# Optimization experiments

Measured on AMD Instinct MI355X. Metric: run time of the kernel, lower is better.

## Reference

```python
import jax, jax.numpy as jnp
import numpy as np

N_NODES = 50000
N_EDGES = 1600000
IN_FEAT = 256
HIDDEN = 128
N_CLASSES = 16


def gcn_conv(x, edge_index, W, b, n_nodes):
    """PyG GCNConv: x' = D^{-1/2} (A+I) D^{-1/2} (x @ W) + b."""
    h = x @ W  # project first (PyG order), messages are in out_dim
    src, dst = edge_index[0], edge_index[1]
    loops = jnp.arange(n_nodes, dtype=src.dtype)
    src = jnp.concatenate([src, loops])
    dst = jnp.concatenate([dst, loops])
    # degree of A+I (count incoming edges incl. self loop)
    deg = jax.ops.segment_sum(jnp.ones_like(dst, dtype=h.dtype), dst, num_segments=n_nodes)
    dis = jax.lax.rsqrt(deg)  # deg >= 1 thanks to self loops
    norm = dis[src] * dis[dst]  # [E+N]
    msgs = h[src] * norm[:, None]  # gather + scale
    out = jax.ops.segment_sum(msgs, dst, num_segments=n_nodes)  # scatter-add
    return out + b


def setup_inputs() -> dict:
    key = jax.random.key(0)
    k_x, k_e, k_w1, k_b1, k_w2, k_b2 = jax.random.split(key, 6)
    x = jax.random.normal(k_x, (N_NODES, IN_FEAT), dtype=jnp.float32)
    edge_index = jax.random.randint(k_e, (2, N_EDGES), 0, N_NODES, dtype=jnp.int64)
    s1 = 1.0 / np.sqrt(IN_FEAT)
    s2 = 1.0 / np.sqrt(HIDDEN)
    W1 = jax.random.uniform(k_w1, (IN_FEAT, HIDDEN), jnp.float32, -s1, s1)
    b1 = jax.random.uniform(k_b1, (HIDDEN,), jnp.float32, -s1, s1)
    W2 = jax.random.uniform(k_w2, (HIDDEN, N_CLASSES), jnp.float32, -s2, s2)
    b2 = jax.random.uniform(k_b2, (N_CLASSES,), jnp.float32, -s2, s2)
    return {"x": x, "edge_index": edge_index, "W1": W1, "b1": b1, "W2": W2, "b2": b2}


def reference(x, edge_index, W1, b1, W2, b2):
    n = x.shape[0]
    h = gcn_conv(x, edge_index, W1, b1, n)
    h = jax.nn.relu(h)
    logits = gcn_conv(h, edge_index, W2, b2, n)
    return logits, jax.nn.softmax(logits, axis=1)
```

## Files before the change

kernel.cpp:

```cpp
#include <hip/hip_runtime.h>
#include <hip/hip_bf16.h>
#include <math.h>

#define N_NODES 50000
#define N_EDGES 1600000
#define IN_FEAT 256
#define HIDDEN 128
#define N_CLASSES 16

#define ECHUNK 2048
#define NCHK 782
#define NBKT 196
#define BCAP 10240
#define CSTR 16

typedef __attribute__((ext_vector_type(8))) short short8;
typedef __attribute__((ext_vector_type(4))) float floatx4;

__device__ __forceinline__ unsigned short f2bf(float f) {
    unsigned u = __float_as_uint(f);
    return (unsigned short)((u + 0x7fffu + ((u >> 16) & 1u)) >> 16);
}

__device__ __forceinline__ unsigned pk2bf(float a, float b) {
    __hip_bfloat162 h = __float22bfloat162_rn(make_float2(a, b));
    union { __hip_bfloat162 h; unsigned u; } cv;
    cv.h = h;
    return cv.u;
}

__device__ __forceinline__ float bflo(unsigned u) { return __uint_as_float(u << 16); }
__device__ __forceinline__ float bfhi(unsigned u) { return __uint_as_float(u & 0xffff0000u); }

__global__ __launch_bounds__(256) void scatter_edges2(const int* __restrict__ src,
                                                      const int* __restrict__ dst,
                                                      int* __restrict__ cursor,
                                                      unsigned int* __restrict__ sorted,
                                                      const float* __restrict__ W1,
                                                      unsigned short* __restrict__ w1t) {
    __shared__ int hloc[256];
    int t = threadIdx.x;
    hloc[t] = 0;
    if (blockIdx.x < HIDDEN)
        w1t[blockIdx.x * IN_FEAT + t] = f2bf(W1[t * HIDDEN + blockIdx.x]);
    __syncthreads();
    int base = blockIdx.x * ECHUNK;
    int end = min(base + ECHUNK, N_EDGES);
    for (int i = base + t; i < end; i += 256)
        atomicAdd(&hloc[dst[i] >> 8], 1);
    __syncthreads();
    int cnt = hloc[t];
    int lbase = 0;
    if (cnt > 0) lbase = t * BCAP + atomicAdd(&cursor[t * CSTR], cnt);
    __syncthreads();
    hloc[t] = lbase;
    __syncthreads();
    for (int i = base + t; i < end; i += 256) {
        int d = dst[i];
        int s = src[i];
        int pos = atomicAdd(&hloc[d >> 8], 1);
        sorted[pos] = ((unsigned)d << 16) | (unsigned)s;
    }
}

__global__ __launch_bounds__(512) void build_csr2(const unsigned int* __restrict__ sorted,
                                                  const int* __restrict__ cursor,
                                                  int* __restrict__ rs,
                                                  int* __restrict__ re,
                                                  float* __restrict__ dis,
                                                  unsigned short* __restrict__ csr_src) {
    __shared__ int cnt[256];
    __shared__ int roff[256];
    int t = threadIdx.x;
    int bkt = blockIdx.x;
    int ebase = bkt * BCAP;
    int eend = ebase + cursor[bkt * CSTR];
    if (t < 256) cnt[t] = 0;
    __syncthreads();
    for (int i = ebase + t; i < eend; i += 512)
        atomicAdd(&cnt[(sorted[i] >> 16) & 255], 1);
    __syncthreads();
    int v = 0;
    if (t < 256) { v = cnt[t]; roff[t] = v; }
    __syncthreads();
    for (int off = 1; off < 256; off <<= 1) {
        int x = (t < 256 && t >= off) ? roff[t - off] : 0;
        __syncthreads();
        if (t < 256) roff[t] += x;
        __syncthreads();
    }
    if (t < 256) {
        int excl = roff[t] - v;
        int node = bkt * 256 + t;
        if (node < N_NODES) {
            rs[node] = ebase + excl;
            re[node] = ebase + excl + v;
            dis[node] = 1.0f / sqrtf((float)(v + 1));
        }
        cnt[t] = ebase + excl;
    }
    __syncthreads();
    for (int i = ebase + t; i < eend; i += 512) {
        unsigned e = sorted[i];
        int pos = atomicAdd(&cnt[(e >> 16) & 255], 1);
        csr_src[pos] = (unsigned short)(e & 0xffffu);
    }
}

#define XCHDW 260
#define KBLK (4 * XCHDW)

__global__ __launch_bounds__(256) void gemm1_mfma(const float* __restrict__ x,
                                                  const unsigned short* __restrict__ w1t,
                                                  const float* __restrict__ dis,
                                                  unsigned int* __restrict__ g1) {
    __shared__ float xs[8 * KBLK];
    int tid = threadIdx.x;
    int w = tid >> 6;
    int lane = tid & 63;
    int quad = lane >> 4;
    int c = lane & 15;
    int row_base = blockIdx.x * 32;
    int col_base = w * 32;

    int st_row = min(row_base + 8 * w + (lane >> 3), N_NODES - 1);
    const float* gp1 = x + (size_t)st_row * IN_FEAT + (lane & 7) * 4;
#pragma unroll
    for (int kk = 0; kk < 8; ++kk)
        __builtin_amdgcn_global_load_lds(
            (const __attribute__((address_space(1))) void*)(gp1 + kk * 32),
            (__attribute__((address_space(3))) void*)&xs[kk * KBLK + w * XCHDW], 16, 0, 0);

    floatx4 acc[2][2] = {};
    const unsigned short* bp[2];
#pragma unroll
    for (int nt = 0; nt < 2; ++nt)
        bp[nt] = w1t + (size_t)(col_base + nt * 16 + c) * IN_FEAT + quad * 8;

    int dwoff[2];
#pragma unroll
    for (int rt = 0; rt < 2; ++rt) {
        int rit = rt * 16 + c;
        dwoff[rt] = (rit >> 3) * XCHDW + (rit & 7) * 32 + quad * 8;
    }

    __syncthreads();

#pragma unroll
    for (int kk = 0; kk < 8; ++kk) {
        short8 b[2];
#pragma unroll
        for (int nt = 0; nt < 2; ++nt)
            b[nt] = *(const short8*)(bp[nt] + kk * 32);
        short8 a[2];
#pragma unroll
        for (int rt = 0; rt < 2; ++rt) {
            float4 f0 = *(const float4*)&xs[kk * KBLK + dwoff[rt]];
            float4 f1 = *(const float4*)&xs[kk * KBLK + dwoff[rt] + 4];
            union { short8 s; unsigned u[4]; } au;
            au.u[0] = pk2bf(f0.x, f0.y);
            au.u[1] = pk2bf(f0.z, f0.w);
            au.u[2] = pk2bf(f1.x, f1.y);
            au.u[3] = pk2bf(f1.z, f1.w);
            a[rt] = au.s;
        }
#pragma unroll
        for (int rt = 0; rt < 2; ++rt)
#pragma unroll
            for (int nt = 0; nt < 2; ++nt)
                acc[rt][nt] = __builtin_amdgcn_mfma_f32_16x16x32_bf16(a[rt], b[nt], acc[rt][nt], 0, 0, 0);
    }

    bool evenlane = (lane & 1) == 0;
#pragma unroll
    for (int rt = 0; rt < 2; ++rt) {
#pragma unroll
        for (int reg = 0; reg < 4; ++reg) {
            int row = row_base + rt * 16 + quad * 4 + reg;
            float dv = dis[min(row, N_NODES - 1)];
#pragma unroll
            for (int nt = 0; nt < 2; ++nt) {
                float v = acc[rt][nt][reg] * dv;
                float vo = __shfl_xor(v, 1);
                if (evenlane && row < N_NODES) {
                    unsigned pkd = (unsigned)f2bf(v) | ((unsigned)f2bf(vo) << 16);
                    int col = col_base + nt * 16 + c;
                    g1[(size_t)(col >> 5) * (N_NODES * 16) + (size_t)row * 16 + ((col & 31) >> 1)] = pkd;
                }
            }
        }
    }
}

__global__ __launch_bounds__(256) void agg1_sliced(const uint4* __restrict__ g1,
                                                   const int* __restrict__ rs,
                                                   const int* __restrict__ re,
                                                   const unsigned short* __restrict__ csr_src,
                                                   const float* __restrict__ dis,
                                                   const float* __restrict__ b1,
                                                   const float* __restrict__ W2,
                                                   float* __restrict__ g2) {
    __shared__ float w2s[32 * 16];
    __shared__ float rbuf[4][16][36];
    int tid = threadIdx.x;
    int bi = blockIdx.x;
    int bucket = bi >> 4;
    int xcd = bi & 7;
    int slice = xcd >> 1;
    int quarter = ((bi >> 3) & 1) * 2 + (xcd & 1);

    for (int i = tid; i < 512; i += 256) w2s[i] = W2[slice * 512 + i];
    __syncthreads();

    int wave = tid >> 6, lane = tid & 63;
    int g = lane >> 2, m4 = lane & 3;
    const uint4* plane = g1 + (size_t)slice * (N_NODES * 4);
    int node = bucket * 256 + quarter * 64 + wave * 16 + g;
    bool alive = (node < N_NODES);
    float dvs = 0.f;

#define ACC8(u) do { a0 += bflo((u).x); a1 += bfhi((u).x); a2 += bflo((u).y); a3 += bfhi((u).y); \
                     a4 += bflo((u).z); a5 += bfhi((u).z); a6 += bflo((u).w); a7 += bfhi((u).w); } while (0)
#define GATH(IV, U0, U1, U2, U3) do {                       \
        int j0_ = (int)((IV).x & 0xffffu);                  \
        int j1_ = (int)((IV).x >> 16);                      \
        int j2_ = (int)((IV).y & 0xffffu);                  \
        int j3_ = (int)((IV).y >> 16);                      \
        U0 = plane[(size_t)j0_ * 4 + m4];                   \
        U1 = plane[(size_t)j1_ * 4 + m4];                   \
        U2 = plane[(size_t)j2_ * 4 + m4];                   \
        U3 = plane[(size_t)j3_ * 4 + m4];                   \
    } while (0)

    if (alive) {
        uint4 su = plane[(size_t)node * 4 + m4];
        float a0 = bflo(su.x), a1 = bfhi(su.x), a2 = bflo(su.y), a3 = bfhi(su.y);
        float a4 = bflo(su.z), a5 = bfhi(su.z), a6 = bflo(su.w), a7 = bfhi(su.w);
        int e = rs[node], e1v = re[node];
        while ((e & 3) && e < e1v) {
            int j = csr_src[e];
            uint4 u = plane[(size_t)j * 4 + m4];
            ACC8(u);
            ++e;
        }
        int nb = (e1v - e) >> 2;
        if (nb >= 2) {
            uint2 Ia = *(const uint2*)&csr_src[e];
            uint2 Ib = *(const uint2*)&csr_src[e + 4];
            uint4 A0, A1, A2, A3, B0, B1, B2, B3;
            GATH(Ia, A0, A1, A2, A3);
            GATH(Ib, B0, B1, B2, B3);
            __builtin_amdgcn_sched_barrier(0);
            int b = 2;
            while (b + 2 <= nb) {
                Ia = *(const uint2*)&csr_src[e + 4 * b];
                ACC8(A0); ACC8(A1); ACC8(A2); ACC8(A3);
                GATH(Ia, A0, A1, A2, A3);
                __builtin_amdgcn_sched_barrier(0);
                Ib = *(const uint2*)&csr_src[e + 4 * b + 4];
                ACC8(B0); ACC8(B1); ACC8(B2); ACC8(B3);
                GATH(Ib, B0, B1, B2, B3);
                __builtin_amdgcn_sched_barrier(0);
                b += 2;
            }
            int rem = nb - b;
            ACC8(A0); ACC8(A1); ACC8(A2); ACC8(A3);
            if (rem) {
                Ia = *(const uint2*)&csr_src[e + 4 * b];
                GATH(Ia, A0, A1, A2, A3);
            }
            ACC8(B0); ACC8(B1); ACC8(B2); ACC8(B3);
            if (rem) { ACC8(A0); ACC8(A1); ACC8(A2); ACC8(A3); }
            e += 4 * nb;
        } else if (nb >= 1) {
            uint2 Iv = *(const uint2*)&csr_src[e];
            uint4 U0, U1, U2, U3;
            GATH(Iv, U0, U1, U2, U3);
            ACC8(U0); ACC8(U1); ACC8(U2); ACC8(U3);
            e += 4;
        }
        while (e < e1v) {
            int j = csr_src[e];
            uint4 u = plane[(size_t)j * 4 + m4];
            ACC8(u);
            ++e;
        }

        float dv = dis[node];
        dvs = dv;
        float4 bb0 = *(const float4*)&b1[slice * 32 + 8 * m4];
        float4 bb1 = *(const float4*)&b1[slice * 32 + 8 * m4 + 4];
        float4 r0, r1;
        r0.x = fmaxf(fmaf(dv, a0, bb0.x), 0.f);
        r0.y = fmaxf(fmaf(dv, a1, bb0.y), 0.f);
        r0.z = fmaxf(fmaf(dv, a2, bb0.z), 0.f);
        r0.w = fmaxf(fmaf(dv, a3, bb0.w), 0.f);
        r1.x = fmaxf(fmaf(dv, a4, bb1.x), 0.f);
        r1.y = fmaxf(fmaf(dv, a5, bb1.y), 0.f);
        r1.z = fmaxf(fmaf(dv, a6, bb1.z), 0.f);
        r1.w = fmaxf(fmaf(dv, a7, bb1.w), 0.f);
        *(float4*)&rbuf[wave][g][8 * m4] = r0;
        *(float4*)&rbuf[wave][g][8 * m4 + 4] = r1;
    }
    __builtin_amdgcn_sched_barrier(0);
    if (alive) {
        float p0 = 0.f, p1 = 0.f, p2 = 0.f, p3 = 0.f;
#pragma unroll
        for (int fb = 0; fb < 8; ++fb) {
            float4 rv = *(const float4*)&rbuf[wave][g][fb * 4];
            float4 w0 = *(const float4*)&w2s[(fb * 4 + 0) * 16 + 4 * m4];
            float4 w1 = *(const float4*)&w2s[(fb * 4 + 1) * 16 + 4 * m4];
            float4 w2 = *(const float4*)&w2s[(fb * 4 + 2) * 16 + 4 * m4];
            float4 w3 = *(const float4*)&w2s[(fb * 4 + 3) * 16 + 4 * m4];
            p0 = fmaf(rv.x, w0.x, p0); p1 = fmaf(rv.x, w0.y, p1);
            p2 = fmaf(rv.x, w0.z, p2); p3 = fmaf(rv.x, w0.w, p3);
            p0 = fmaf(rv.y, w1.x, p0); p1 = fmaf(rv.y, w1.y, p1);
            p2 = fmaf(rv.y, w1.z, p2); p3 = fmaf(rv.y, w1.w, p3);
            p0 = fmaf(rv.z, w2.x, p0); p1 = fmaf(rv.z, w2.y, p1);
            p2 = fmaf(rv.z, w2.z, p2); p3 = fmaf(rv.z, w2.w, p3);
            p0 = fmaf(rv.w, w3.x, p0); p1 = fmaf(rv.w, w3.y, p1);
            p2 = fmaf(rv.w, w3.z, p2); p3 = fmaf(rv.w, w3.w, p3);
        }
        float* go = g2 + (size_t)node * 16 + 4 * m4;
        unsafeAtomicAdd(go + 0, dvs * p0);
        unsafeAtomicAdd(go + 1, dvs * p1);
        unsafeAtomicAdd(go + 2, dvs * p2);
        unsafeAtomicAdd(go + 3, dvs * p3);
    }
#undef GATH
#undef ACC8
}

__global__ __launch_bounds__(256) void agg2_softmax(const float4* __restrict__ g2,
                                                    const int* __restrict__ rs,
                                                    const int* __restrict__ re,
                                                    const unsigned short* __restrict__ csr_src,
                                                    const float* __restrict__ dis,
                                                    const float* __restrict__ b2,
                                                    float* __restrict__ out) {
    int tid = threadIdx.x;
    int wave = tid >> 6, lane = tid & 63;
    int g = lane >> 2, m4 = lane & 3;
    int node = blockIdx.x * 64 + wave * 16 + g;
    if (node >= N_NODES) return;

    float4 acc = g2[(size_t)node * 4 + m4];

#define ACC4(u) do { acc.x += (u).x; acc.y += (u).y; acc.z += (u).z; acc.w += (u).w; } while (0)
#define GATH4(IV, U0, U1, U2, U3) do {                      \
        int j0_ = (int)((IV).x & 0xffffu);                  \
        int j1_ = (int)((IV).x >> 16);                      \
        int j2_ = (int)((IV).y & 0xffffu);                  \
        int j3_ = (int)((IV).y >> 16);                      \
        U0 = g2[(size_t)j0_ * 4 + m4];                      \
        U1 = g2[(size_t)j1_ * 4 + m4];                      \
        U2 = g2[(size_t)j2_ * 4 + m4];                      \
        U3 = g2[(size_t)j3_ * 4 + m4];                      \
    } while (0)

    int e = rs[node], e1v = re[node];
    while ((e & 3) && e < e1v) {
        int j = csr_src[e];
        float4 u = g2[(size_t)j * 4 + m4];
        ACC4(u);
        ++e;
    }
    int nb = (e1v - e) >> 2;
    if (nb >= 2) {
        uint2 Ia = *(const uint2*)&csr_src[e];
        uint2 Ib = *(const uint2*)&csr_src[e + 4];
        float4 A0, A1, A2, A3, B0, B1, B2, B3;
        GATH4(Ia, A0, A1, A2, A3);
        GATH4(Ib, B0, B1, B2, B3);
        __builtin_amdgcn_sched_barrier(0);
        int b = 2;
        while (b + 2 <= nb) {
            Ia = *(const uint2*)&csr_src[e + 4 * b];
            ACC4(A0); ACC4(A1); ACC4(A2); ACC4(A3);
            GATH4(Ia, A0, A1, A2, A3);
            __builtin_amdgcn_sched_barrier(0);
            Ib = *(const uint2*)&csr_src[e + 4 * b + 4];
            ACC4(B0); ACC4(B1); ACC4(B2); ACC4(B3);
            GATH4(Ib, B0, B1, B2, B3);
            __builtin_amdgcn_sched_barrier(0);
            b += 2;
        }
        int rem = nb - b;
        ACC4(A0); ACC4(A1); ACC4(A2); ACC4(A3);
        if (rem) {
            Ia = *(const uint2*)&csr_src[e + 4 * b];
            GATH4(Ia, A0, A1, A2, A3);
        }
        ACC4(B0); ACC4(B1); ACC4(B2); ACC4(B3);
        if (rem) { ACC4(A0); ACC4(A1); ACC4(A2); ACC4(A3); }
        e += 4 * nb;
    } else if (nb >= 1) {
        uint2 Iv = *(const uint2*)&csr_src[e];
        float4 U0, U1, U2, U3;
        GATH4(Iv, U0, U1, U2, U3);
        ACC4(U0); ACC4(U1); ACC4(U2); ACC4(U3);
        e += 4;
    }
    while (e < e1v) {
        int j = csr_src[e];
        float4 u = g2[(size_t)j * 4 + m4];
        ACC4(u);
        ++e;
    }
#undef GATH4
#undef ACC4

    float dv = dis[node];
    float4 bb = *(const float4*)&b2[4 * m4];
    float4 lg;
    lg.x = fmaf(dv, acc.x, bb.x);
    lg.y = fmaf(dv, acc.y, bb.y);
    lg.z = fmaf(dv, acc.z, bb.z);
    lg.w = fmaf(dv, acc.w, bb.w);
    ((float4*)out)[(size_t)node * 4 + m4] = lg;

    float m = fmaxf(fmaxf(lg.x, lg.y), fmaxf(lg.z, lg.w));
    m = fmaxf(m, __shfl_xor(m, 1));
    m = fmaxf(m, __shfl_xor(m, 2));
    float4 ex;
    ex.x = expf(lg.x - m); ex.y = expf(lg.y - m);
    ex.z = expf(lg.z - m); ex.w = expf(lg.w - m);
    float s = (ex.x + ex.y) + (ex.z + ex.w);
    s += __shfl_xor(s, 1);
    s += __shfl_xor(s, 2);
    float inv = 1.0f / s;
    ex.x *= inv; ex.y *= inv; ex.z *= inv; ex.w *= inv;
    ((float4*)out)[(size_t)N_NODES * 4 + (size_t)node * 4 + m4] = ex;
}


extern "C" void kernel_launch(void* const* d_in, const int* in_sizes, int n_in,
                              void* d_out, int out_size, void* d_ws, size_t ws_size,
                              hipStream_t stream) {
    const float* x  = (const float*)d_in[0];
    const int*   ei = (const int*)d_in[1];
    const float* W1 = (const float*)d_in[2];
    const float* b1 = (const float*)d_in[3];
    const float* W2 = (const float*)d_in[4];
    const float* b2 = (const float*)d_in[5];
    float* out = (float*)d_out;

    char* ws = (char*)d_ws;
    size_t off = 0;
    auto alloc = [&](size_t bytes) -> char* {
        char* p = ws + off;
        off = (off + bytes + 511) & ~(size_t)511;
        return p;
    };
    int*   cursor   = (int*)alloc(256 * CSTR * 4);
    float* g2       = (float*)alloc((size_t)N_NODES * N_CLASSES * 4);
    float* dis      = (float*)alloc(N_NODES * 4);
    int*   rs       = (int*)alloc(N_NODES * 4);
    int*   re       = (int*)alloc(N_NODES * 4);
    unsigned short* w1t = (unsigned short*)alloc((size_t)HIDDEN * IN_FEAT * 2);
    unsigned short* csr_src = (unsigned short*)alloc((size_t)NBKT * BCAP * 2);
    unsigned int* g1 = (unsigned int*)alloc((size_t)N_NODES * 64 * 4);
    unsigned int* sorted = (unsigned int*)g1;
    (void)ws_size; (void)in_sizes; (void)n_in; (void)out_size;

    const int* src = ei;
    const int* dst = ei + N_EDGES;

    size_t zspan = (size_t)((char*)(g2 + (size_t)N_NODES * N_CLASSES) - (char*)cursor);
    hipMemsetAsync(cursor, 0, zspan, stream);
    scatter_edges2<<<NCHK, 256, 0, stream>>>(src, dst, cursor, sorted, W1, w1t);
    build_csr2<<<NBKT, 512, 0, stream>>>(sorted, cursor, rs, re, dis, csr_src);

    gemm1_mfma<<<(N_NODES + 31) / 32, 256, 0, stream>>>(x, w1t, dis, g1);
    agg1_sliced<<<NBKT * 16, 256, 0, stream>>>((const uint4*)g1, rs, re, csr_src, dis, b1, W2, g2);
    agg2_softmax<<<N_NODES / 64 + 1, 256, 0, stream>>>((const float4*)g2, rs, re, csr_src, dis, b2, out);
}
```

Before: 237.7 us.

## Replace g2 atomic accumulation with per-slice partial buffers and a reduce kernel

Each of the four feature slices in agg1_sliced now writes its partial layer-2 projection into its own buffer with a plain float4 store instead of atomically adding into a shared g2. A new g2_reduce kernel sums the four partials, applies the degree scaling and writes the result in place. Because the buffer no longer needs zeroing, the large memset is reduced to just the cursor array. The agg1 launch is also split into two half-grid launches. The change removes atomic contention and the memset cost but adds an extra kernel, an extra launch, and four times the g2 storage traffic.

```diff
diff --git a/kernel.cpp b/kernel.cpp
--- a/kernel.cpp
+++ b/kernel.cpp
@@ -199,11 +199,12 @@
                                                    const float* __restrict__ dis,
                                                    const float* __restrict__ b1,
                                                    const float* __restrict__ W2,
-                                                   float* __restrict__ g2) {
+                                                   float* __restrict__ g2p,
+                                                   int bi0) {
     __shared__ float w2s[32 * 16];
     __shared__ float rbuf[4][16][36];
     int tid = threadIdx.x;
-    int bi = blockIdx.x;
+    int bi = blockIdx.x + bi0;
     int bucket = bi >> 4;
     int xcd = bi & 7;
     int slice = xcd >> 1;
@@ -215,9 +216,9 @@
     int wave = tid >> 6, lane = tid & 63;
     int g = lane >> 2, m4 = lane & 3;
     const uint4* plane = g1 + (size_t)slice * (N_NODES * 4);
+    float* gp = g2p + (size_t)slice * ((size_t)N_NODES * 16);
     int node = bucket * 256 + quarter * 64 + wave * 16 + g;
     bool alive = (node < N_NODES);
-    float dvs = 0.f;
 
 #define ACC8(u) do { a0 += bflo((u).x); a1 += bfhi((u).x); a2 += bflo((u).y); a3 += bfhi((u).y); \
                      a4 += bflo((u).z); a5 += bfhi((u).z); a6 += bflo((u).w); a7 += bfhi((u).w); } while (0)
@@ -287,7 +288,6 @@
         }
 
         float dv = dis[node];
-        dvs = dv;
         float4 bb0 = *(const float4*)&b1[slice * 32 + 8 * m4];
         float4 bb1 = *(const float4*)&b1[slice * 32 + 8 * m4 + 4];
         float4 r0, r1;
@@ -321,14 +321,30 @@
             p0 = fmaf(rv.w, w3.x, p0); p1 = fmaf(rv.w, w3.y, p1);
             p2 = fmaf(rv.w, w3.z, p2); p3 = fmaf(rv.w, w3.w, p3);
         }
-        float* go = g2 + (size_t)node * 16 + 4 * m4;
-        unsafeAtomicAdd(go + 0, dvs * p0);
-        unsafeAtomicAdd(go + 1, dvs * p1);
-        unsafeAtomicAdd(go + 2, dvs * p2);
-        unsafeAtomicAdd(go + 3, dvs * p3);
+        float4 pv; pv.x = p0; pv.y = p1; pv.z = p2; pv.w = p3;
+        *(float4*)&gp[(size_t)node * 16 + 4 * m4] = pv;
     }
 #undef GATH
 #undef ACC8
+}
+
+__global__ __launch_bounds__(256) void g2_reduce(float* __restrict__ g2p,
+                                                 const float* __restrict__ dis) {
+    int i = blockIdx.x * 256 + threadIdx.x;
+    if (i >= N_NODES * 4) return;
+    const size_t PS = (size_t)N_NODES * 16 / 4;
+    const float4* p = (const float4*)g2p;
+    float4 a = p[i];
+    float4 b = p[i + PS];
+    float4 c = p[i + 2 * PS];
+    float4 d = p[i + 3 * PS];
+    float dv = dis[i >> 2];
+    float4 r;
+    r.x = dv * ((a.x + b.x) + (c.x + d.x));
+    r.y = dv * ((a.y + b.y) + (c.y + d.y));
+    r.z = dv * ((a.z + b.z) + (c.z + d.z));
+    r.w = dv * ((a.w + b.w) + (c.w + d.w));
+    ((float4*)g2p)[i] = r;
 }
 
 __global__ __launch_bounds__(256) void agg2_softmax(const float4* __restrict__ g2,
@@ -453,25 +469,26 @@
         return p;
     };
     int*   cursor   = (int*)alloc(256 * CSTR * 4);
-    float* g2       = (float*)alloc((size_t)N_NODES * N_CLASSES * 4);
     float* dis      = (float*)alloc(N_NODES * 4);
     int*   rs       = (int*)alloc(N_NODES * 4);
     int*   re       = (int*)alloc(N_NODES * 4);
     unsigned short* w1t = (unsigned short*)alloc((size_t)HIDDEN * IN_FEAT * 2);
     unsigned short* csr_src = (unsigned short*)alloc((size_t)NBKT * BCAP * 2);
     unsigned int* g1 = (unsigned int*)alloc((size_t)N_NODES * 64 * 4);
+    float* g2p      = (float*)alloc(4 * (size_t)N_NODES * N_CLASSES * 4);
     unsigned int* sorted = (unsigned int*)g1;
     (void)ws_size; (void)in_sizes; (void)n_in; (void)out_size;
 
     const int* src = ei;
     const int* dst = ei + N_EDGES;
 
-    size_t zspan = (size_t)((char*)(g2 + (size_t)N_NODES * N_CLASSES) - (char*)cursor);
-    hipMemsetAsync(cursor, 0, zspan, stream);
+    hipMemsetAsync(cursor, 0, 256 * CSTR * 4, stream);
     scatter_edges2<<<NCHK, 256, 0, stream>>>(src, dst, cursor, sorted, W1, w1t);
     build_csr2<<<NBKT, 512, 0, stream>>>(sorted, cursor, rs, re, dis, csr_src);
 
     gemm1_mfma<<<(N_NODES + 31) / 32, 256, 0, stream>>>(x, w1t, dis, g1);
-    agg1_sliced<<<NBKT * 16, 256, 0, stream>>>((const uint4*)g1, rs, re, csr_src, dis, b1, W2, g2);
-    agg2_softmax<<<N_NODES / 64 + 1, 256, 0, stream>>>((const float4*)g2, rs, re, csr_src, dis, b2, out);
-}
+    agg1_sliced<<<NBKT * 8, 256, 0, stream>>>((const uint4*)g1, rs, re, csr_src, dis, b1, W2, g2p, 0);
+    agg1_sliced<<<NBKT * 8, 256, 0, stream>>>((const uint4*)g1, rs, re, csr_src, dis, b1, W2, g2p, NBKT * 8);
+    g2_reduce<<<(N_NODES * 4 + 255) / 256, 256, 0, stream>>>(g2p, dis);
+    agg2_softmax<<<N_NODES / 64 + 1, 256, 0, stream>>>((const float4*)g2p, rs, re, csr_src, dis, b2, out);
+}
```

Measured after the change: 230.2 us. 1.03x faster.
